# Performance work log

Measured on AMD Instinct MI355X. Metric: run time of the kernel, lower is better.

Reference implementation:

```python
import jax, jax.numpy as jnp
import numpy as np

N_NODES = 100000
N_EDGES = 1250000
IN_CH = 64
HID = 64
OUT_CH = 8
N_GRAPHS = 512


def _gcn_conv(x, W, b, src, dst, n):
    """PyG GCNConv: add self-loops, symmetric deg^-1/2 normalization, scatter-add."""
    h = x @ W  # [N, F_out]
    ones = jnp.ones(src.shape, dtype=h.dtype)
    deg = jax.ops.segment_sum(ones, dst, num_segments=n) + 1.0  # +1 for self-loop
    dinv = jax.lax.rsqrt(deg)
    coef = (dinv[src] * dinv[dst])[:, None]          # [E,1]
    agg = jax.ops.segment_sum(h[src] * coef, dst, num_segments=n)  # neighbor msgs
    self_term = h * (dinv * dinv)[:, None]           # self-loop msg, norm = 1/deg
    return agg + self_term + b


def setup_inputs() -> dict:
    key = jax.random.key(0)
    ks = jax.random.split(key, 8)
    x = jax.random.normal(ks[0], (N_NODES, IN_CH), dtype=jnp.float32)
    edge_index = jax.random.randint(ks[1], (2, N_EDGES), 0, N_NODES, dtype=jnp.int64)
    batch = jnp.sort(jax.random.randint(ks[2], (N_NODES,), 0, N_GRAPHS, dtype=jnp.int64))
    s = 0.1
    W0 = jax.random.normal(ks[3], (IN_CH, HID), dtype=jnp.float32) * s
    W1 = jax.random.normal(ks[4], (HID, HID), dtype=jnp.float32) * s
    W2 = jax.random.normal(ks[5], (HID, HID), dtype=jnp.float32) * s
    Wfc = jax.random.normal(ks[6], (HID, OUT_CH), dtype=jnp.float32) * s
    b0 = jnp.zeros((HID,), dtype=jnp.float32)
    b1 = jnp.zeros((HID,), dtype=jnp.float32)
    b2 = jnp.zeros((HID,), dtype=jnp.float32)
    bfc = jnp.zeros((OUT_CH,), dtype=jnp.float32)
    return {"x": x, "edge_index": edge_index, "batch": batch,
            "W0": W0, "b0": b0, "W1": W1, "b1": b1, "W2": W2, "b2": b2,
            "Wfc": Wfc, "bfc": bfc}


def reference(x, edge_index, batch, W0, b0, W1, b1, W2, b2, Wfc, bfc):
    src, dst = edge_index[0], edge_index[1]
    n = x.shape[0]
    h = jax.nn.relu(_gcn_conv(x, W0, b0, src, dst, n))
    h = jax.nn.relu(_gcn_conv(h, W1, b1, src, dst, n))
    h = jax.nn.relu(_gcn_conv(h, W2, b2, src, dst, n))
    # global_mean_pool over graph ids
    sums = jax.ops.segment_sum(h, batch, num_segments=N_GRAPHS)  # [G, HID]
    cnt = jax.ops.segment_sum(jnp.ones((n,), dtype=h.dtype), batch, num_segments=N_GRAPHS)
    pooled = sums / jnp.maximum(cnt, 1.0)[:, None]
    return jax.nn.sigmoid(pooled @ Wfc + bfc)  # [G, OUT_CH]
```

## Files before the change

### kernel.cpp

```cpp
#include <hip/hip_runtime.h>
#include <math.h>


#define FEAT 64
#define CAP 40
#define EDGE_BLOCKS 2048

typedef _Float16 half4 __attribute__((ext_vector_type(4)));
typedef float floatx2 __attribute__((ext_vector_type(2)));


__global__ void k_zero(int* __restrict__ p, int n, float* __restrict__ q, int m) {
    int i = blockIdx.x * blockDim.x + threadIdx.x;
    if (i < n) p[i] = 0;
    if (i < m) q[i] = 0.f;
}


__global__ void k_scatter(const int* __restrict__ ei, int* __restrict__ ecnt,
                          int* __restrict__ csr, int E, int N) {
    int g = blockIdx.x & 7;
    int bi = blockIdx.x >> 3;
    int lo = (int)((long long)N * g >> 3);
    int hi = (int)((long long)N * (g + 1) >> 3);
    for (int base = bi * 1024; base < E; base += (EDGE_BLOCKS / 8) * 1024) {
        int e0 = base + threadIdx.x;
        #pragma unroll
        for (int k = 0; k < 4; ++k) {
            int e = e0 + k * 256;
            if (e < E) {
                int d = ei[E + e];
                if (d >= lo && d < hi) {
                    int s = ei[e];
                    int slot = atomicAdd(&ecnt[d], 1);
                    if (slot < CAP) csr[(size_t)d * CAP + slot] = s;
                }
            }
        }
    }
}


template<typename T>
__global__ __launch_bounds__(256, 2)
void k_matmul(const T* __restrict__ X, const float* __restrict__ W,
              const int* __restrict__ ecnt, unsigned int* __restrict__ h8,
              int n) {
    __shared__ float Ws[FEAT][68];
    __shared__ float Xs[FEAT][68];
    int tid = threadIdx.x;
    int cidx = tid & 15;
    int ridx = tid >> 4;
    int rowbase = blockIdx.x << 6;

    const float4* Wg4 = (const float4*)W;
    for (int idx = tid; idx < FEAT * 16; idx += 256) {
        int k = idx >> 4, p = idx & 15;
        *(float4*)&Ws[k][p << 2] = Wg4[idx];
    }
    for (int idx = tid; idx < FEAT * 16; idx += 256) {
        int r = idx >> 4, p = idx & 15;
        int row = rowbase + r;
        float4 v = make_float4(0.f, 0.f, 0.f, 0.f);
        if (row < n) {
            if constexpr (sizeof(T) == 4) {
                v = ((const float4*)X)[(size_t)row * 16 + p];
            } else {
                half4 hv = ((const half4*)X)[(size_t)row * 16 + p];
                v = make_float4((float)hv.x, (float)hv.y, (float)hv.z, (float)hv.w);
            }
        }
        *(float4*)&Xs[r][p << 2] = v;
    }
    __syncthreads();

    int r0 = ridx << 2;
    int c0 = cidx << 2;
    float4 a0 = make_float4(0.f, 0.f, 0.f, 0.f);
    float4 a1 = a0, a2 = a0, a3 = a0;
    #pragma unroll 2
    for (int k = 0; k < FEAT; k += 4) {
        float4 w0 = *(const float4*)&Ws[k + 0][c0];
        float4 w1 = *(const float4*)&Ws[k + 1][c0];
        float4 w2 = *(const float4*)&Ws[k + 2][c0];
        float4 w3 = *(const float4*)&Ws[k + 3][c0];
        float4 x0 = *(const float4*)&Xs[r0 + 0][k];
        float4 x1 = *(const float4*)&Xs[r0 + 1][k];
        float4 x2 = *(const float4*)&Xs[r0 + 2][k];
        float4 x3 = *(const float4*)&Xs[r0 + 3][k];
        a0.x += x0.x*w0.x + x0.y*w1.x + x0.z*w2.x + x0.w*w3.x;
        a0.y += x0.x*w0.y + x0.y*w1.y + x0.z*w2.y + x0.w*w3.y;
        a0.z += x0.x*w0.z + x0.y*w1.z + x0.z*w2.z + x0.w*w3.z;
        a0.w += x0.x*w0.w + x0.y*w1.w + x0.z*w2.w + x0.w*w3.w;
        a1.x += x1.x*w0.x + x1.y*w1.x + x1.z*w2.x + x1.w*w3.x;
        a1.y += x1.x*w0.y + x1.y*w1.y + x1.z*w2.y + x1.w*w3.y;
        a1.z += x1.x*w0.z + x1.y*w1.z + x1.z*w2.z + x1.w*w3.z;
        a1.w += x1.x*w0.w + x1.y*w1.w + x1.z*w2.w + x1.w*w3.w;
        a2.x += x2.x*w0.x + x2.y*w1.x + x2.z*w2.x + x2.w*w3.x;
        a2.y += x2.x*w0.y + x2.y*w1.y + x2.z*w2.y + x2.w*w3.y;
        a2.z += x2.x*w0.z + x2.y*w1.z + x2.z*w2.z + x2.w*w3.z;
        a2.w += x2.x*w0.w + x2.y*w1.w + x2.z*w2.w + x2.w*w3.w;
        a3.x += x3.x*w0.x + x3.y*w1.x + x3.z*w2.x + x3.w*w3.x;
        a3.y += x3.x*w0.y + x3.y*w1.y + x3.z*w2.y + x3.w*w3.y;
        a3.z += x3.x*w0.z + x3.y*w1.z + x3.z*w2.z + x3.w*w3.z;
        a3.w += x3.x*w0.w + x3.y*w1.w + x3.z*w2.w + x3.w*w3.w;
    }
    int row0 = rowbase + r0;
    #pragma unroll
    for (int r = 0; r < 4; ++r) {
        int row = row0 + r;
        if (row < n) {
            float4 a = (r == 0) ? a0 : (r == 1) ? a1 : (r == 2) ? a2 : a3;
            float dv = rsqrtf((float)ecnt[row] + 1.0f);
            unsigned int p = 0;
            p = __builtin_amdgcn_cvt_pk_fp8_f32(a.x * dv, a.y * dv, p, false);
            p = __builtin_amdgcn_cvt_pk_fp8_f32(a.z * dv, a.w * dv, p, true);
            h8[(size_t)row * 16 + cidx] = p;
        }
    }
}


__global__ void k_agg(const int* __restrict__ ecnt, const int* __restrict__ csr,
                      const unsigned int* __restrict__ h8,
                      const float* __restrict__ b, _Float16* __restrict__ out, int N) {
    int tid = blockIdx.x * blockDim.x + threadIdx.x;
    int node = tid >> 4;
    int fq = tid & 15;
    if (node >= N) return;
    int deg = ecnt[node];
    if (deg > CAP) deg = CAP;
    size_t off0 = (size_t)node * CAP;
    float4 acc = make_float4(0.f, 0.f, 0.f, 0.f);
    int j = 0;
    for (; j + 4 <= deg; j += 4) {
        int s0 = csr[off0 + j];
        int s1 = csr[off0 + j + 1];
        int s2 = csr[off0 + j + 2];
        int s3 = csr[off0 + j + 3];
        unsigned int u0 = h8[(size_t)s0 * 16 + fq];
        unsigned int u1 = h8[(size_t)s1 * 16 + fq];
        unsigned int u2 = h8[(size_t)s2 * 16 + fq];
        unsigned int u3 = h8[(size_t)s3 * 16 + fq];
        floatx2 l0 = __builtin_amdgcn_cvt_pk_f32_fp8(u0, false);
        floatx2 h0 = __builtin_amdgcn_cvt_pk_f32_fp8(u0, true);
        floatx2 l1 = __builtin_amdgcn_cvt_pk_f32_fp8(u1, false);
        floatx2 h1 = __builtin_amdgcn_cvt_pk_f32_fp8(u1, true);
        floatx2 l2 = __builtin_amdgcn_cvt_pk_f32_fp8(u2, false);
        floatx2 h2 = __builtin_amdgcn_cvt_pk_f32_fp8(u2, true);
        floatx2 l3 = __builtin_amdgcn_cvt_pk_f32_fp8(u3, false);
        floatx2 h3 = __builtin_amdgcn_cvt_pk_f32_fp8(u3, true);
        acc.x += (l0.x + l1.x) + (l2.x + l3.x);
        acc.y += (l0.y + l1.y) + (l2.y + l3.y);
        acc.z += (h0.x + h1.x) + (h2.x + h3.x);
        acc.w += (h0.y + h1.y) + (h2.y + h3.y);
    }
    for (; j < deg; ++j) {
        unsigned int u = h8[(size_t)csr[off0 + j] * 16 + fq];
        floatx2 l = __builtin_amdgcn_cvt_pk_f32_fp8(u, false);
        floatx2 hh = __builtin_amdgcn_cvt_pk_f32_fp8(u, true);
        acc.x += l.x; acc.y += l.y; acc.z += hh.x; acc.w += hh.y;
    }
    unsigned int uo = h8[(size_t)node * 16 + fq];
    floatx2 ol = __builtin_amdgcn_cvt_pk_f32_fp8(uo, false);
    floatx2 oh = __builtin_amdgcn_cvt_pk_f32_fp8(uo, true);
    float4 bb = *(const float4*)&b[fq << 2];
    float dv = rsqrtf((float)deg + 1.0f);
    half4 r;
    r.x = (_Float16)fmaxf(dv * (acc.x + ol.x) + bb.x, 0.f);
    r.y = (_Float16)fmaxf(dv * (acc.y + ol.y) + bb.y, 0.f);
    r.z = (_Float16)fmaxf(dv * (acc.z + oh.x) + bb.z, 0.f);
    r.w = (_Float16)fmaxf(dv * (acc.w + oh.y) + bb.w, 0.f);
    *(half4*)&out[(size_t)node * FEAT + (fq << 2)] = r;
}


#define PCH 64
__global__ void k_pool(const _Float16* __restrict__ h, const int* __restrict__ batch,
                       float* __restrict__ pooled, float* __restrict__ gcnt, int N) {
    int wave = blockIdx.x * (blockDim.x >> 6) + (threadIdx.x >> 6);
    int f = threadIdx.x & 63;
    int start = wave * PCH;
    if (start >= N) return;
    int end = start + PCH; if (end > N) end = N;
    int cur = batch[start];
    float acc = 0.f;
    int nl = 0;
    for (int i = start; i < end; ++i) {
        int g = batch[i];
        if (g != cur) {
            atomicAdd(&pooled[(size_t)cur * FEAT + f], acc);
            if (f == 0) atomicAdd(&gcnt[cur], (float)nl);
            cur = g; acc = 0.f; nl = 0;
        }
        acc += (float)h[(size_t)i * FEAT + f];
        nl++;
    }
    atomicAdd(&pooled[(size_t)cur * FEAT + f], acc);
    if (f == 0) atomicAdd(&gcnt[cur], (float)nl);
}

__global__ void k_fc_sigmoid(const float* __restrict__ pooled, const float* __restrict__ gcnt,
                             const float* __restrict__ Wfc, const float* __restrict__ bfc,
                             float* __restrict__ out, int G) {
    __shared__ float P[FEAT];
    int g = blockIdx.x;
    int t = threadIdx.x;
    float c = fmaxf(gcnt[g], 1.0f);
    P[t] = pooled[(size_t)g * FEAT + t] / c;
    __syncthreads();
    if (t < 8) {
        float acc = bfc[t];
        #pragma unroll
        for (int f = 0; f < FEAT; ++f) acc += P[f] * Wfc[f * 8 + t];
        out[(size_t)g * 8 + t] = 1.f / (1.f + expf(-acc));
    }
}


extern "C" void kernel_launch(void* const* d_in, const int* in_sizes, int n_in,
                              void* d_out, int out_size, void* d_ws, size_t ws_size,
                              hipStream_t stream) {
    const float* x    = (const float*)d_in[0];
    const int*   ei   = (const int*)d_in[1];
    const int*   batch= (const int*)d_in[2];
    const float* W0   = (const float*)d_in[3];
    const float* b0   = (const float*)d_in[4];
    const float* W1   = (const float*)d_in[5];
    const float* b1   = (const float*)d_in[6];
    const float* W2   = (const float*)d_in[7];
    const float* b2   = (const float*)d_in[8];
    const float* Wfc  = (const float*)d_in[9];
    const float* bfc  = (const float*)d_in[10];
    float* out = (float*)d_out;

    const int N = in_sizes[0] / FEAT;
    const int E = in_sizes[1] / 2;
    const int G = out_size / 8;

    _Float16* bufA  = (_Float16*)d_ws;
    _Float16* bufB  = bufA + (size_t)N * FEAT;
    unsigned int* h8 = (unsigned int*)(bufB + (size_t)N * FEAT);
    float* pooled   = (float*)(h8 + (size_t)N * 16);
    float* gcnt     = pooled + (size_t)G * FEAT;
    int*   ecnt     = (int*)(gcnt + G);
    int*   csr      = ecnt + N;

    const int TB = 256;
    dim3 blk(TB);
    dim3 gN((N + TB - 1) / TB);
    dim3 gEP(EDGE_BLOCKS);
    dim3 gAgg(((size_t)N * 16 + TB - 1) / TB);
    dim3 gMM((N + 63) / 64);

    k_zero<<<gN, blk, 0, stream>>>(ecnt, N, pooled, G * (FEAT + 1));
    k_scatter<<<gEP, blk, 0, stream>>>(ei, ecnt, csr, E, N);

    k_matmul<float><<<gMM, blk, 0, stream>>>(x, W0, ecnt, h8, N);
    k_agg<<<gAgg, blk, 0, stream>>>(ecnt, csr, h8, b0, bufA, N);
    k_matmul<_Float16><<<gMM, blk, 0, stream>>>(bufA, W1, ecnt, h8, N);
    k_agg<<<gAgg, blk, 0, stream>>>(ecnt, csr, h8, b1, bufB, N);
    k_matmul<_Float16><<<gMM, blk, 0, stream>>>(bufB, W2, ecnt, h8, N);
    k_agg<<<gAgg, blk, 0, stream>>>(ecnt, csr, h8, b2, bufA, N);

    k_pool<<<dim3(((N + PCH - 1) / PCH + 3) / 4), blk, 0, stream>>>(bufA, batch, pooled, gcnt, N);
    k_fc_sigmoid<<<dim3(G), dim3(FEAT), 0, stream>>>(pooled, gcnt, Wfc, bfc, out, G);
}
```

Before: 235.6 us.

## Use f16 MFMA for the dense feature transform in k_matmul

Replaces the FP32 FMA register-tiled 64x64 matmul with MFMA 16x16x32 f16 instructions, staging X and a transposed W as f16 in shared memory. Results are written back through shared memory so the existing fp8 packing and deg^-1/2 scaling epilogue stays unchanged. Launch bounds are raised to allow 4 blocks per CU, since shared memory use shrinks. This cuts ALU work in the matmul, but rounding inputs to f16 adds precision loss, and the extra syncs and LDS round trip add some cost. The aggregation kernels likely dominate total time anyway.

Result: faster. 209.0 us (-11.3%).

```diff
diff --git a/kernel.cpp b/kernel.cpp
--- a/kernel.cpp
+++ b/kernel.cpp
@@ -7,7 +7,9 @@
 #define EDGE_BLOCKS 2048
 
 typedef _Float16 half4 __attribute__((ext_vector_type(4)));
+typedef _Float16 f16x8 __attribute__((ext_vector_type(8)));
 typedef float floatx2 __attribute__((ext_vector_type(2)));
+typedef float f32x4 __attribute__((ext_vector_type(4)));
 
 
 __global__ void k_zero(int* __restrict__ p, int n, float* __restrict__ q, int m) {
@@ -42,80 +44,99 @@
 
 
 template<typename T>
-__global__ __launch_bounds__(256, 2)
+__global__ __launch_bounds__(256, 4)
 void k_matmul(const T* __restrict__ X, const float* __restrict__ W,
               const int* __restrict__ ecnt, unsigned int* __restrict__ h8,
               int n) {
-    __shared__ float Ws[FEAT][68];
-    __shared__ float Xs[FEAT][68];
+    __shared__ __align__(16) char smem[2 * 64 * 72 * 2];
+    _Float16 (*Xh)[72] = (_Float16(*)[72])smem;
+    _Float16 (*Wt)[72] = (_Float16(*)[72])(smem + 64 * 72 * 2);
+    float (*Df)[68] = (float(*)[68])smem;
+
     int tid = threadIdx.x;
-    int cidx = tid & 15;
-    int ridx = tid >> 4;
     int rowbase = blockIdx.x << 6;
 
-    const float4* Wg4 = (const float4*)W;
-    for (int idx = tid; idx < FEAT * 16; idx += 256) {
-        int k = idx >> 4, p = idx & 15;
-        *(float4*)&Ws[k][p << 2] = Wg4[idx];
-    }
-    for (int idx = tid; idx < FEAT * 16; idx += 256) {
-        int r = idx >> 4, p = idx & 15;
-        int row = rowbase + r;
-        float4 v = make_float4(0.f, 0.f, 0.f, 0.f);
-        if (row < n) {
-            if constexpr (sizeof(T) == 4) {
-                v = ((const float4*)X)[(size_t)row * 16 + p];
-            } else {
-                half4 hv = ((const half4*)X)[(size_t)row * 16 + p];
-                v = make_float4((float)hv.x, (float)hv.y, (float)hv.z, (float)hv.w);
-            }
-        }
-        *(float4*)&Xs[r][p << 2] = v;
-    }
-    __syncthreads();
-
-    int r0 = ridx << 2;
-    int c0 = cidx << 2;
-    float4 a0 = make_float4(0.f, 0.f, 0.f, 0.f);
-    float4 a1 = a0, a2 = a0, a3 = a0;
-    #pragma unroll 2
-    for (int k = 0; k < FEAT; k += 4) {
-        float4 w0 = *(const float4*)&Ws[k + 0][c0];
-        float4 w1 = *(const float4*)&Ws[k + 1][c0];
-        float4 w2 = *(const float4*)&Ws[k + 2][c0];
-        float4 w3 = *(const float4*)&Ws[k + 3][c0];
-        float4 x0 = *(const float4*)&Xs[r0 + 0][k];
-        float4 x1 = *(const float4*)&Xs[r0 + 1][k];
-        float4 x2 = *(const float4*)&Xs[r0 + 2][k];
-        float4 x3 = *(const float4*)&Xs[r0 + 3][k];
-        a0.x += x0.x*w0.x + x0.y*w1.x + x0.z*w2.x + x0.w*w3.x;
-        a0.y += x0.x*w0.y + x0.y*w1.y + x0.z*w2.y + x0.w*w3.y;
-        a0.z += x0.x*w0.z + x0.y*w1.z + x0.z*w2.z + x0.w*w3.z;
-        a0.w += x0.x*w0.w + x0.y*w1.w + x0.z*w2.w + x0.w*w3.w;
-        a1.x += x1.x*w0.x + x1.y*w1.x + x1.z*w2.x + x1.w*w3.x;
-        a1.y += x1.x*w0.y + x1.y*w1.y + x1.z*w2.y + x1.w*w3.y;
-        a1.z += x1.x*w0.z + x1.y*w1.z + x1.z*w2.z + x1.w*w3.z;
-        a1.w += x1.x*w0.w + x1.y*w1.w + x1.z*w2.w + x1.w*w3.w;
-        a2.x += x2.x*w0.x + x2.y*w1.x + x2.z*w2.x + x2.w*w3.x;
-        a2.y += x2.x*w0.y + x2.y*w1.y + x2.z*w2.y + x2.w*w3.y;
-        a2.z += x2.x*w0.z + x2.y*w1.z + x2.z*w2.z + x2.w*w3.z;
-        a2.w += x2.x*w0.w + x2.y*w1.w + x2.z*w2.w + x2.w*w3.w;
-        a3.x += x3.x*w0.x + x3.y*w1.x + x3.z*w2.x + x3.w*w3.x;
-        a3.y += x3.x*w0.y + x3.y*w1.y + x3.z*w2.y + x3.w*w3.y;
-        a3.z += x3.x*w0.z + x3.y*w1.z + x3.z*w2.z + x3.w*w3.z;
-        a3.w += x3.x*w0.w + x3.y*w1.w + x3.z*w2.w + x3.w*w3.w;
-    }
-    int row0 = rowbase + r0;
+    for (int idx = tid; idx < 64 * 16; idx += 256) {
+        int k = idx >> 4, p = (idx & 15) << 2;
+        float4 w = *(const float4*)&W[k * 64 + p];
+        Wt[p + 0][k] = (_Float16)w.x;
+        Wt[p + 1][k] = (_Float16)w.y;
+        Wt[p + 2][k] = (_Float16)w.z;
+        Wt[p + 3][k] = (_Float16)w.w;
+    }
+    if constexpr (sizeof(T) == 4) {
+        for (int idx = tid; idx < 64 * 16; idx += 256) {
+            int r = idx >> 4, p = (idx & 15) << 2;
+            int row = rowbase + r;
+            float4 v = make_float4(0.f, 0.f, 0.f, 0.f);
+            if (row < n) v = *(const float4*)&X[(size_t)row * FEAT + p];
+            Xh[r][p + 0] = (_Float16)v.x;
+            Xh[r][p + 1] = (_Float16)v.y;
+            Xh[r][p + 2] = (_Float16)v.z;
+            Xh[r][p + 3] = (_Float16)v.w;
+        }
+    } else {
+        for (int idx = tid; idx < 64 * 8; idx += 256) {
+            int r = idx >> 3, p = (idx & 7) << 3;
+            int row = rowbase + r;
+            f16x8 v = {};
+            if (row < n) v = *(const f16x8*)&X[(size_t)row * FEAT + p];
+            *(f16x8*)&Xh[r][p] = v;
+        }
+    }
+    __syncthreads();
+
+    int wv = tid >> 6;
+    int l = tid & 63;
+    int m16 = l & 15;
+    int kg = l >> 4;
+    int wrow = wv << 4;
+
+    f16x8 a0 = *(const f16x8*)&Xh[wrow + m16][kg * 8];
+    f16x8 a1 = *(const f16x8*)&Xh[wrow + m16][32 + kg * 8];
+    f32x4 c0 = {}, c1 = {}, c2 = {}, c3 = {};
+    f16x8 b;
+    b = *(const f16x8*)&Wt[ 0 + m16][kg * 8];
+    c0 = __builtin_amdgcn_mfma_f32_16x16x32_f16(a0, b, c0, 0, 0, 0);
+    b = *(const f16x8*)&Wt[ 0 + m16][32 + kg * 8];
+    c0 = __builtin_amdgcn_mfma_f32_16x16x32_f16(a1, b, c0, 0, 0, 0);
+    b = *(const f16x8*)&Wt[16 + m16][kg * 8];
+    c1 = __builtin_amdgcn_mfma_f32_16x16x32_f16(a0, b, c1, 0, 0, 0);
+    b = *(const f16x8*)&Wt[16 + m16][32 + kg * 8];
+    c1 = __builtin_amdgcn_mfma_f32_16x16x32_f16(a1, b, c1, 0, 0, 0);
+    b = *(const f16x8*)&Wt[32 + m16][kg * 8];
+    c2 = __builtin_amdgcn_mfma_f32_16x16x32_f16(a0, b, c2, 0, 0, 0);
+    b = *(const f16x8*)&Wt[32 + m16][32 + kg * 8];
+    c2 = __builtin_amdgcn_mfma_f32_16x16x32_f16(a1, b, c2, 0, 0, 0);
+    b = *(const f16x8*)&Wt[48 + m16][kg * 8];
+    c3 = __builtin_amdgcn_mfma_f32_16x16x32_f16(a0, b, c3, 0, 0, 0);
+    b = *(const f16x8*)&Wt[48 + m16][32 + kg * 8];
+    c3 = __builtin_amdgcn_mfma_f32_16x16x32_f16(a1, b, c3, 0, 0, 0);
+
+    __syncthreads();
+
     #pragma unroll
     for (int r = 0; r < 4; ++r) {
-        int row = row0 + r;
+        int lr = wrow + kg * 4 + r;
+        Df[lr][ 0 + m16] = c0[r];
+        Df[lr][16 + m16] = c1[r];
+        Df[lr][32 + m16] = c2[r];
+        Df[lr][48 + m16] = c3[r];
+    }
+    __syncthreads();
+
+    int r0 = (tid >> 4) << 2;
+    int c4 = tid & 15;
+    #pragma unroll
+    for (int r = 0; r < 4; ++r) {
+        int row = rowbase + r0 + r;
         if (row < n) {
-            float4 a = (r == 0) ? a0 : (r == 1) ? a1 : (r == 2) ? a2 : a3;
+            float4 a = *(float4*)&Df[r0 + r][c4 << 2];
             float dv = rsqrtf((float)ecnt[row] + 1.0f);
             unsigned int p = 0;
             p = __builtin_amdgcn_cvt_pk_fp8_f32(a.x * dv, a.y * dv, p, false);
             p = __builtin_amdgcn_cvt_pk_fp8_f32(a.z * dv, a.w * dv, p, true);
-            h8[(size_t)row * 16 + cidx] = p;
+            h8[(size_t)row * 16 + c4] = p;
         }
     }
 }
```
